# Kernel optimization log

Measured on AMD Instinct MI355X. Metric: run time of the kernel, lower is better.

## Reference

```python
import jax, jax.numpy as jnp
import numpy as np
import math

SEQ, BATCH, IN_DIM = 2048, 2, 512
EMBED, HEADS = 512, 8
HEAD_DIM = EMBED // HEADS


def setup_inputs() -> dict:
    key = jax.random.key(0)
    ks = jax.random.split(key, 6)
    # xavier-uniform style init for weights (stored as [in, out])
    def xavier(k, fan_in, fan_out):
        limit = math.sqrt(6.0 / (fan_in + fan_out))
        return jax.random.uniform(k, (fan_in, fan_out), jnp.float32, -limit, limit)
    return {
        "x": jax.random.normal(ks[0], (SEQ, BATCH, IN_DIM), jnp.float32),
        "relative_positional_bias": jax.random.normal(ks[1], (1, HEADS, SEQ, SEQ), jnp.float32),
        "Wqkv": xavier(ks[2], IN_DIM, 3 * EMBED),
        "bqkv": jnp.zeros((3 * EMBED,), jnp.float32),
        "Wo": xavier(ks[3], EMBED, EMBED),
        "bo": jnp.zeros((EMBED,), jnp.float32),
    }


def reference(x, relative_positional_bias, Wqkv, bqkv, Wo, bo):
    # x: [S, B, D] -> [B, S, D]
    xb = jnp.transpose(x, (1, 0, 2))
    B, S, _ = xb.shape
    qkv = xb @ Wqkv + bqkv                       # [B, S, 3E]
    qkv = qkv.reshape(B, S, HEADS, 3 * HEAD_DIM).transpose(0, 2, 1, 3)  # [B,H,S,3hd]
    q, k, v = jnp.split(qkv, 3, axis=-1)         # each [B, H, S, hd]
    # nonstandard scaling: 1/sqrt(2 * d_k)
    scale = 1.0 / math.sqrt(2.0 * HEAD_DIM)
    logits = jnp.einsum("bhqd,bhkd->bhqk", q, k) * scale
    logits = logits + relative_positional_bias   # broadcast over batch
    attn = jax.nn.softmax(logits, axis=-1)
    vals = jnp.einsum("bhqk,bhkd->bhqd", attn, v)  # [B, H, S, hd]
    vals = vals.transpose(0, 2, 1, 3).reshape(B, S, EMBED)
    return vals @ Wo + bo                        # [B, S, E]
```

## Files before the change

### kernel.cpp

```cpp
#include <hip/hip_runtime.h>
#include <hip/hip_bf16.h>

#define SEQ 2048
#define BATCH 2
#define IN_DIM 512
#define EMBED 512
#define HEADS 8
#define HD 64
#define N3 1536

using f32x4 = __attribute__((ext_vector_type(4))) float;
using s16x8 = __attribute__((ext_vector_type(8))) short;

__device__ __forceinline__ unsigned short f2bf(float f) {
    union { float f; unsigned int u; } v; v.f = f;
    unsigned int u = v.u;
    unsigned int r = (u + 0x7FFFu + ((u >> 16) & 1u)) >> 16;
    return (unsigned short)r;
}

__global__ __launch_bounds__(256) void prep_x(
    const float* __restrict__ x, unsigned short* __restrict__ Ab)
{
    const int gid = blockIdx.x * 256 + threadIdx.x;
    const int base = gid * 4;
    const int m = base >> 9, k = base & 511;
    const int b = m >> 11, s = m & 2047;
    float4 f = *reinterpret_cast<const float4*>(x + ((size_t)s * BATCH + b) * IN_DIM + k);
    ushort4 u;
    u.x = f2bf(f.x); u.y = f2bf(f.y); u.z = f2bf(f.z); u.w = f2bf(f.w);
    *reinterpret_cast<ushort4*>(Ab + (size_t)m * IN_DIM + k) = u;
}

__global__ __launch_bounds__(256) void transpose_w(
    const float* __restrict__ in, unsigned short* __restrict__ out, int K, int N)
{
    __shared__ __align__(16) unsigned short T[64][72];
    const int k0 = blockIdx.x * 64, n0 = blockIdx.y * 64;
    const int tid = threadIdx.x;
    const int ri = tid >> 2, cj = (tid & 3) * 16;
#pragma unroll
    for (int v = 0; v < 4; v++) {
        float4 f = *reinterpret_cast<const float4*>(in + (size_t)(k0 + ri) * N + n0 + cj + 4 * v);
        T[cj + 4 * v + 0][ri] = f2bf(f.x);
        T[cj + 4 * v + 1][ri] = f2bf(f.y);
        T[cj + 4 * v + 2][ri] = f2bf(f.z);
        T[cj + 4 * v + 3][ri] = f2bf(f.w);
    }
    __syncthreads();
    unsigned short* dst = out + (size_t)(n0 + ri) * K + k0 + cj;
    *reinterpret_cast<uint4*>(dst)     = *reinterpret_cast<const uint4*>(&T[ri][cj]);
    *reinterpret_cast<uint4*>(dst + 8) = *reinterpret_cast<const uint4*>(&T[ri][cj + 8]);
}

__global__ __launch_bounds__(256) void qkv_proj(
    const unsigned short* __restrict__ Ab, const unsigned short* __restrict__ Wt,
    const float* __restrict__ bqkv,
    unsigned short* __restrict__ Qb, unsigned short* __restrict__ Kb,
    unsigned short* __restrict__ Vt)
{
    __shared__ __align__(16) unsigned short As[64][72];
    __shared__ __align__(16) unsigned short Bs[64][72];
    const int bm = blockIdx.x, bn = blockIdx.y;
    const int tid = threadIdx.x;
    const int lane = tid & 63, w = tid >> 6;
    const int fr = lane & 15, fg = lane >> 4;
    const int m0 = bm * 64, n0 = bn * 64;
    const int ri = tid >> 2, cj = (tid & 3) * 16;

    f32x4 acc[4];
#pragma unroll
    for (int t = 0; t < 4; t++) acc[t] = (f32x4){0.f, 0.f, 0.f, 0.f};

    for (int k0 = 0; k0 < IN_DIM; k0 += 64) {
        const unsigned short* asrc = Ab + (size_t)(m0 + ri) * IN_DIM + k0 + cj;
        *reinterpret_cast<uint4*>(&As[ri][cj])     = *reinterpret_cast<const uint4*>(asrc);
        *reinterpret_cast<uint4*>(&As[ri][cj + 8]) = *reinterpret_cast<const uint4*>(asrc + 8);
        const unsigned short* bsrc = Wt + (size_t)(n0 + ri) * IN_DIM + k0 + cj;
        *reinterpret_cast<uint4*>(&Bs[ri][cj])     = *reinterpret_cast<const uint4*>(bsrc);
        *reinterpret_cast<uint4*>(&Bs[ri][cj + 8]) = *reinterpret_cast<const uint4*>(bsrc + 8);
        __syncthreads();
#pragma unroll
        for (int h2 = 0; h2 < 2; h2++) {
            s16x8 a = *reinterpret_cast<const s16x8*>(&As[w * 16 + fr][h2 * 32 + fg * 8]);
#pragma unroll
            for (int t = 0; t < 4; t++) {
                s16x8 b = *reinterpret_cast<const s16x8*>(&Bs[t * 16 + fr][h2 * 32 + fg * 8]);
                acc[t] = __builtin_amdgcn_mfma_f32_16x16x32_bf16(a, b, acc[t], 0, 0, 0);
            }
        }
        __syncthreads();
    }

    const int h = bn / 3, route = bn % 3;
    const int b_ = m0 >> 11, s0 = m0 & 2047;
    if (route < 2) {
        unsigned short* dst = (route == 0) ? Qb : Kb;
#pragma unroll
        for (int t = 0; t < 4; t++) {
            const int d = t * 16 + fr;
            const float bq = bqkv[n0 + t * 16 + fr];
#pragma unroll
            for (int j = 0; j < 4; j++) {
                const int sl = s0 + w * 16 + fg * 4 + j;
                dst[(((size_t)b_ * HEADS + h) * SEQ + sl) * HD + d] = f2bf(acc[t][j] + bq);
            }
        }
    } else {
#pragma unroll
        for (int t = 0; t < 4; t++) {
            const float bq = bqkv[n0 + t * 16 + fr];
#pragma unroll
            for (int j = 0; j < 4; j++)
                As[t * 16 + fr][w * 16 + fg * 4 + j] = f2bf(acc[t][j] + bq);
        }
        __syncthreads();
        unsigned short* dst = Vt + (((size_t)b_ * HEADS + h) * HD + ri) * SEQ + s0 + cj;
        *reinterpret_cast<uint4*>(dst)     = *reinterpret_cast<const uint4*>(&As[ri][cj]);
        *reinterpret_cast<uint4*>(dst + 8) = *reinterpret_cast<const uint4*>(&As[ri][cj + 8]);
    }
}

__global__ __launch_bounds__(256) void flash_attn(
    const unsigned short* __restrict__ Qb, const unsigned short* __restrict__ Kb,
    const unsigned short* __restrict__ Vt, const float* __restrict__ bias,
    unsigned short* __restrict__ Ob)
{
    __shared__ __align__(16) unsigned short Ks[2][64][72];
    __shared__ __align__(16) unsigned short Vs[2][64][72];
    __shared__ __align__(16) unsigned short Ps[4][16][72];
    const int h = blockIdx.y, b = blockIdx.z;
    const int q0 = blockIdx.x * 64;
    const int tid = threadIdx.x, lane = tid & 63, w = tid >> 6;
    const int fr = lane & 15, fg = lane >> 4;

    const unsigned short* Kbase = Kb + (size_t)(b * HEADS + h) * SEQ * HD;
    const unsigned short* Vbase = Vt + (size_t)(b * HEADS + h) * HD * SEQ;
    const float* bbase = bias + (size_t)h * SEQ * SEQ + (size_t)q0 * SEQ;

    const unsigned short* qrow = Qb + ((size_t)(b * HEADS + h) * SEQ + q0 + w * 16 + fr) * HD;
    s16x8 qf0 = *reinterpret_cast<const s16x8*>(qrow + fg * 8);
    s16x8 qf1 = *reinterpret_cast<const s16x8*>(qrow + 32 + fg * 8);

    const int r0 = tid >> 3, c0 = (tid & 7) * 8;
    const int r1 = r0 + 32;

    uint4 kr0, kr1, vr0, vr1;
    float bA[4][4], bB[4][4];

    kr0 = *reinterpret_cast<const uint4*>(Kbase + (size_t)r0 * HD + c0);
    kr1 = *reinterpret_cast<const uint4*>(Kbase + (size_t)r1 * HD + c0);
    vr0 = *reinterpret_cast<const uint4*>(Vbase + (size_t)r0 * SEQ + c0);
    vr1 = *reinterpret_cast<const uint4*>(Vbase + (size_t)r1 * SEQ + c0);
#pragma unroll
    for (int t = 0; t < 4; t++)
#pragma unroll
        for (int j = 0; j < 4; j++)
            bA[t][j] = bbase[(size_t)(w * 16 + fg * 4 + j) * SEQ + t * 16 + fr];
    *reinterpret_cast<uint4*>(&Ks[0][r0][c0]) = kr0;
    *reinterpret_cast<uint4*>(&Ks[0][r1][c0]) = kr1;
    *reinterpret_cast<uint4*>(&Vs[0][r0][c0]) = vr0;
    *reinterpret_cast<uint4*>(&Vs[0][r1][c0]) = vr1;
    __syncthreads();

    float mrow[4], lrow[4];
    f32x4 oacc[4];
#pragma unroll
    for (int j = 0; j < 4; j++) { mrow[j] = -1e30f; lrow[j] = 0.f; }
#pragma unroll
    for (int t = 0; t < 4; t++) oacc[t] = (f32x4){0.f, 0.f, 0.f, 0.f};

    const float scale = 0.08838834764831845f;

    auto body = [&](int n, const float (&bc)[4][4], float (&bnx)[4][4]) {
        const int cur = n & 1;
        const bool pf = (n < 31);
        const int kn = (n + 1) * 64;
        if (pf) {
            kr0 = *reinterpret_cast<const uint4*>(Kbase + (size_t)(kn + r0) * HD + c0);
            kr1 = *reinterpret_cast<const uint4*>(Kbase + (size_t)(kn + r1) * HD + c0);
            vr0 = *reinterpret_cast<const uint4*>(Vbase + (size_t)r0 * SEQ + kn + c0);
            vr1 = *reinterpret_cast<const uint4*>(Vbase + (size_t)r1 * SEQ + kn + c0);
#pragma unroll
            for (int t = 0; t < 4; t++)
#pragma unroll
                for (int j = 0; j < 4; j++)
                    bnx[t][j] = bbase[(size_t)(w * 16 + fg * 4 + j) * SEQ + kn + t * 16 + fr];
        }
        f32x4 sacc[4];
#pragma unroll
        for (int t = 0; t < 4; t++) sacc[t] = (f32x4){0.f, 0.f, 0.f, 0.f};
#pragma unroll
        for (int h2 = 0; h2 < 2; h2++) {
            s16x8 a = (h2 == 0) ? qf0 : qf1;
#pragma unroll
            for (int t = 0; t < 4; t++) {
                s16x8 kf = *reinterpret_cast<const s16x8*>(&Ks[cur][t * 16 + fr][h2 * 32 + fg * 8]);
                sacc[t] = __builtin_amdgcn_mfma_f32_16x16x32_bf16(a, kf, sacc[t], 0, 0, 0);
            }
        }
#pragma unroll
        for (int t = 0; t < 4; t++)
#pragma unroll
            for (int j = 0; j < 4; j++)
                sacc[t][j] = sacc[t][j] * scale + bc[t][j];
        float fac[4];
#pragma unroll
        for (int j = 0; j < 4; j++) {
            float m = fmaxf(fmaxf(sacc[0][j], sacc[1][j]), fmaxf(sacc[2][j], sacc[3][j]));
#pragma unroll
            for (int msk = 1; msk < 16; msk <<= 1) m = fmaxf(m, __shfl_xor(m, msk, 64));
            const float newm = fmaxf(mrow[j], m);
            fac[j] = __expf(mrow[j] - newm);
            mrow[j] = newm;
        }
#pragma unroll
        for (int t = 0; t < 4; t++)
#pragma unroll
            for (int j = 0; j < 4; j++)
                sacc[t][j] = __expf(sacc[t][j] - mrow[j]);
#pragma unroll
        for (int j = 0; j < 4; j++) {
            float s = sacc[0][j] + sacc[1][j] + sacc[2][j] + sacc[3][j];
#pragma unroll
            for (int msk = 1; msk < 16; msk <<= 1) s += __shfl_xor(s, msk, 64);
            lrow[j] = lrow[j] * fac[j] + s;
        }
#pragma unroll
        for (int t = 0; t < 4; t++)
#pragma unroll
            for (int j = 0; j < 4; j++)
                Ps[w][fg * 4 + j][t * 16 + fr] = f2bf(sacc[t][j]);
#pragma unroll
        for (int t = 0; t < 4; t++)
#pragma unroll
            for (int j = 0; j < 4; j++)
                oacc[t][j] *= fac[j];
#pragma unroll
        for (int h2 = 0; h2 < 2; h2++) {
            s16x8 pa = *reinterpret_cast<const s16x8*>(&Ps[w][fr][h2 * 32 + fg * 8]);
#pragma unroll
            for (int t = 0; t < 4; t++) {
                s16x8 vf = *reinterpret_cast<const s16x8*>(&Vs[cur][t * 16 + fr][h2 * 32 + fg * 8]);
                oacc[t] = __builtin_amdgcn_mfma_f32_16x16x32_bf16(pa, vf, oacc[t], 0, 0, 0);
            }
        }
        if (pf) {
            const int nxt = cur ^ 1;
            *reinterpret_cast<uint4*>(&Ks[nxt][r0][c0]) = kr0;
            *reinterpret_cast<uint4*>(&Ks[nxt][r1][c0]) = kr1;
            *reinterpret_cast<uint4*>(&Vs[nxt][r0][c0]) = vr0;
            *reinterpret_cast<uint4*>(&Vs[nxt][r1][c0]) = vr1;
        }
        __syncthreads();
    };

    for (int n = 0; n < 32; n += 2) {
        body(n, bA, bB);
        body(n + 1, bB, bA);
    }

#pragma unroll
    for (int t = 0; t < 4; t++)
#pragma unroll
        for (int j = 0; j < 4; j++) {
            const int grow = q0 + w * 16 + fg * 4 + j;
            const float o = oacc[t][j] / lrow[j];
            Ob[((size_t)b * SEQ + grow) * EMBED + h * HD + t * 16 + fr] = f2bf(o);
        }
}

__global__ __launch_bounds__(256) void out_proj(
    const unsigned short* __restrict__ Ao, const unsigned short* __restrict__ Wot,
    const float* __restrict__ bo, float* __restrict__ out)
{
    __shared__ __align__(16) unsigned short As[64][72];
    __shared__ __align__(16) unsigned short Bs[64][72];
    const int bm = blockIdx.x, bn = blockIdx.y;
    const int tid = threadIdx.x, lane = tid & 63, w = tid >> 6;
    const int fr = lane & 15, fg = lane >> 4;
    const int m0 = bm * 64, n0 = bn * 64;
    const int ri = tid >> 2, cj = (tid & 3) * 16;

    f32x4 acc[4];
#pragma unroll
    for (int t = 0; t < 4; t++) acc[t] = (f32x4){0.f, 0.f, 0.f, 0.f};

    for (int k0 = 0; k0 < EMBED; k0 += 64) {
        const unsigned short* asrc = Ao + (size_t)(m0 + ri) * EMBED + k0 + cj;
        *reinterpret_cast<uint4*>(&As[ri][cj])     = *reinterpret_cast<const uint4*>(asrc);
        *reinterpret_cast<uint4*>(&As[ri][cj + 8]) = *reinterpret_cast<const uint4*>(asrc + 8);
        const unsigned short* bsrc = Wot + (size_t)(n0 + ri) * EMBED + k0 + cj;
        *reinterpret_cast<uint4*>(&Bs[ri][cj])     = *reinterpret_cast<const uint4*>(bsrc);
        *reinterpret_cast<uint4*>(&Bs[ri][cj + 8]) = *reinterpret_cast<const uint4*>(bsrc + 8);
        __syncthreads();
#pragma unroll
        for (int h2 = 0; h2 < 2; h2++) {
            s16x8 a = *reinterpret_cast<const s16x8*>(&As[w * 16 + fr][h2 * 32 + fg * 8]);
#pragma unroll
            for (int t = 0; t < 4; t++) {
                s16x8 b = *reinterpret_cast<const s16x8*>(&Bs[t * 16 + fr][h2 * 32 + fg * 8]);
                acc[t] = __builtin_amdgcn_mfma_f32_16x16x32_bf16(a, b, acc[t], 0, 0, 0);
            }
        }
        __syncthreads();
    }

#pragma unroll
    for (int t = 0; t < 4; t++) {
        const int col = n0 + t * 16 + fr;
        const float bb = bo[col];
#pragma unroll
        for (int j = 0; j < 4; j++) {
            const int grow = m0 + w * 16 + fg * 4 + j;
            out[(size_t)grow * EMBED + col] = acc[t][j] + bb;
        }
    }
}

extern "C" void kernel_launch(void* const* d_in, const int* in_sizes, int n_in,
                              void* d_out, int out_size, void* d_ws, size_t ws_size,
                              hipStream_t stream) {
    const float* x    = (const float*)d_in[0];
    const float* bias = (const float*)d_in[1];
    const float* Wqkv = (const float*)d_in[2];
    const float* bqkv = (const float*)d_in[3];
    const float* Wo   = (const float*)d_in[4];
    const float* bo   = (const float*)d_in[5];
    float* out = (float*)d_out;

    const size_t perT = (size_t)BATCH * HEADS * SEQ * HD;
    unsigned short* Qb    = (unsigned short*)d_ws;
    unsigned short* Kb    = Qb + perT;
    unsigned short* Vt    = Kb + perT;
    unsigned short* Ob    = Vt + perT;
    unsigned short* Ab    = Ob + perT;
    unsigned short* Wqkvt = Ab + (size_t)BATCH * SEQ * IN_DIM;
    unsigned short* Wot   = Wqkvt + (size_t)N3 * IN_DIM;

    prep_x<<<2048, 256, 0, stream>>>(x, Ab);
    transpose_w<<<dim3(8, 24), 256, 0, stream>>>(Wqkv, Wqkvt, IN_DIM, N3);
    transpose_w<<<dim3(8, 8), 256, 0, stream>>>(Wo, Wot, EMBED, EMBED);
    qkv_proj<<<dim3(64, 24), 256, 0, stream>>>(Ab, Wqkvt, bqkv, Qb, Kb, Vt);
    flash_attn<<<dim3(32, 8, 2), 256, 0, stream>>>(Qb, Kb, Vt, bias, Ob);
    out_proj<<<dim3(64, 8), 256, 0, stream>>>(Ob, Wot, bo, out);
}
```

Before: 266.1 us.

## Split attention KV range across blocks, async-LDS GEMMs, transposed score MFMA

Flash attention can now split the key range in two, doubling the grid, and a combine kernel merges the partial outputs using the saved row max and sum. The score and PV MFMAs swap operands so each lane owns one query row, which allows vectorised bias loads and cuts the shuffle reductions. The QKV and output GEMMs move to 64x128 tiles filled with global_load_lds and an XOR-swizzled LDS layout, and the two weight transposes merge into one launch. The split path runs only when the workspace is large enough, and it adds fp32 partial traffic plus an extra kernel launch.

```diff
diff --git a/kernel.cpp b/kernel.cpp
--- a/kernel.cpp
+++ b/kernel.cpp
@@ -17,6 +17,12 @@
     unsigned int u = v.u;
     unsigned int r = (u + 0x7FFFu + ((u >> 16) & 1u)) >> 16;
     return (unsigned short)r;
+}
+
+__device__ __forceinline__ void async16(void* lds, const void* g) {
+    __builtin_amdgcn_global_load_lds(
+        (const __attribute__((address_space(1))) unsigned int*)g,
+        (__attribute__((address_space(3))) unsigned int*)lds, 16, 0, 0);
 }
 
 __global__ __launch_bounds__(256) void prep_x(
@@ -32,11 +38,16 @@
     *reinterpret_cast<ushort4*>(Ab + (size_t)m * IN_DIM + k) = u;
 }
 
-__global__ __launch_bounds__(256) void transpose_w(
-    const float* __restrict__ in, unsigned short* __restrict__ out, int K, int N)
+__global__ __launch_bounds__(256) void transpose_w2(
+    const float* __restrict__ Wqkv, const float* __restrict__ Wo,
+    unsigned short* __restrict__ Wqkvt, unsigned short* __restrict__ Wot)
 {
     __shared__ __align__(16) unsigned short T[64][72];
-    const int k0 = blockIdx.x * 64, n0 = blockIdx.y * 64;
+    const int yy = blockIdx.y;
+    const float* in; unsigned short* out; int N, n0;
+    if (yy < 24) { in = Wqkv; out = Wqkvt; N = N3;    n0 = yy * 64; }
+    else         { in = Wo;   out = Wot;   N = EMBED; n0 = (yy - 24) * 64; }
+    const int k0 = blockIdx.x * 64;
     const int tid = threadIdx.x;
     const int ri = tid >> 2, cj = (tid & 3) * 16;
 #pragma unroll
@@ -48,88 +59,120 @@
         T[cj + 4 * v + 3][ri] = f2bf(f.w);
     }
     __syncthreads();
-    unsigned short* dst = out + (size_t)(n0 + ri) * K + k0 + cj;
+    unsigned short* dst = out + (size_t)(n0 + ri) * IN_DIM + k0 + cj;
     *reinterpret_cast<uint4*>(dst)     = *reinterpret_cast<const uint4*>(&T[ri][cj]);
     *reinterpret_cast<uint4*>(dst + 8) = *reinterpret_cast<const uint4*>(&T[ri][cj + 8]);
 }
 
-__global__ __launch_bounds__(256) void qkv_proj(
+__global__ __launch_bounds__(256) void qkv_gemm(
     const unsigned short* __restrict__ Ab, const unsigned short* __restrict__ Wt,
     const float* __restrict__ bqkv,
     unsigned short* __restrict__ Qb, unsigned short* __restrict__ Kb,
     unsigned short* __restrict__ Vt)
 {
-    __shared__ __align__(16) unsigned short As[64][72];
-    __shared__ __align__(16) unsigned short Bs[64][72];
-    const int bm = blockIdx.x, bn = blockIdx.y;
-    const int tid = threadIdx.x;
-    const int lane = tid & 63, w = tid >> 6;
+    __shared__ __align__(16) unsigned short As[64 * 64];
+    __shared__ __align__(16) unsigned short Bs[128 * 64];
+    const int tid = threadIdx.x, lane = tid & 63, w = tid >> 6;
     const int fr = lane & 15, fg = lane >> 4;
-    const int m0 = bm * 64, n0 = bn * 64;
-    const int ri = tid >> 2, cj = (tid & 3) * 16;
-
-    f32x4 acc[4];
-#pragma unroll
-    for (int t = 0; t < 4; t++) acc[t] = (f32x4){0.f, 0.f, 0.f, 0.f};
+    const int m0 = blockIdx.x * 64, n0 = blockIdx.y * 128;
+    const int sr = lane >> 3;
+    const int scs = ((lane & 7) * 16) ^ (sr << 4);
+
+    const unsigned char* Ag = (const unsigned char*)Ab + (size_t)(m0 + w * 8 + sr) * 1024 + scs;
+    const unsigned char* Bg = (const unsigned char*)Wt + (size_t)(n0 + w * 8 + sr) * 1024 + scs;
+    unsigned char* Asb = (unsigned char*)As;
+    unsigned char* Bsb = (unsigned char*)Bs;
+
+    f32x4 acc[2][4];
+#pragma unroll
+    for (int mt = 0; mt < 2; mt++)
+#pragma unroll
+        for (int nt = 0; nt < 4; nt++) acc[mt][nt] = (f32x4){0.f, 0.f, 0.f, 0.f};
+
+    const int swz = (fr & 7) << 4;
 
     for (int k0 = 0; k0 < IN_DIM; k0 += 64) {
-        const unsigned short* asrc = Ab + (size_t)(m0 + ri) * IN_DIM + k0 + cj;
-        *reinterpret_cast<uint4*>(&As[ri][cj])     = *reinterpret_cast<const uint4*>(asrc);
-        *reinterpret_cast<uint4*>(&As[ri][cj + 8]) = *reinterpret_cast<const uint4*>(asrc + 8);
-        const unsigned short* bsrc = Wt + (size_t)(n0 + ri) * IN_DIM + k0 + cj;
-        *reinterpret_cast<uint4*>(&Bs[ri][cj])     = *reinterpret_cast<const uint4*>(bsrc);
-        *reinterpret_cast<uint4*>(&Bs[ri][cj + 8]) = *reinterpret_cast<const uint4*>(bsrc + 8);
+        async16(Asb + (w * 8) * 128,        Ag);
+        async16(Asb + (32 + w * 8) * 128,   Ag + (size_t)32 * 1024);
+        async16(Bsb + (w * 8) * 128,        Bg);
+        async16(Bsb + (32 + w * 8) * 128,   Bg + (size_t)32 * 1024);
+        async16(Bsb + (64 + w * 8) * 128,   Bg + (size_t)64 * 1024);
+        async16(Bsb + (96 + w * 8) * 128,   Bg + (size_t)96 * 1024);
+        Ag += 128; Bg += 128;
         __syncthreads();
 #pragma unroll
         for (int h2 = 0; h2 < 2; h2++) {
-            s16x8 a = *reinterpret_cast<const s16x8*>(&As[w * 16 + fr][h2 * 32 + fg * 8]);
-#pragma unroll
-            for (int t = 0; t < 4; t++) {
-                s16x8 b = *reinterpret_cast<const s16x8*>(&Bs[t * 16 + fr][h2 * 32 + fg * 8]);
-                acc[t] = __builtin_amdgcn_mfma_f32_16x16x32_bf16(a, b, acc[t], 0, 0, 0);
-            }
+            const int cb = (h2 * 64 + fg * 16) ^ swz;
+            s16x8 a[2], bf[4];
+#pragma unroll
+            for (int mt = 0; mt < 2; mt++) {
+                const int row = (w >> 1) * 32 + mt * 16 + fr;
+                a[mt] = *reinterpret_cast<const s16x8*>(Asb + row * 128 + cb);
+            }
+#pragma unroll
+            for (int nt = 0; nt < 4; nt++) {
+                const int nrow = (w & 1) * 64 + nt * 16 + fr;
+                bf[nt] = *reinterpret_cast<const s16x8*>(Bsb + nrow * 128 + cb);
+            }
+#pragma unroll
+            for (int mt = 0; mt < 2; mt++)
+#pragma unroll
+                for (int nt = 0; nt < 4; nt++)
+                    acc[mt][nt] = __builtin_amdgcn_mfma_f32_16x16x32_bf16(a[mt], bf[nt], acc[mt][nt], 0, 0, 0);
         }
         __syncthreads();
     }
 
-    const int h = bn / 3, route = bn % 3;
-    const int b_ = m0 >> 11, s0 = m0 & 2047;
-    if (route < 2) {
-        unsigned short* dst = (route == 0) ? Qb : Kb;
-#pragma unroll
-        for (int t = 0; t < 4; t++) {
-            const int d = t * 16 + fr;
-            const float bq = bqkv[n0 + t * 16 + fr];
-#pragma unroll
-            for (int j = 0; j < 4; j++) {
-                const int sl = s0 + w * 16 + fg * 4 + j;
-                dst[(((size_t)b_ * HEADS + h) * SEQ + sl) * HD + d] = f2bf(acc[t][j] + bq);
-            }
-        }
-    } else {
-#pragma unroll
-        for (int t = 0; t < 4; t++) {
-            const float bq = bqkv[n0 + t * 16 + fr];
-#pragma unroll
-            for (int j = 0; j < 4; j++)
-                As[t * 16 + fr][w * 16 + fg * 4 + j] = f2bf(acc[t][j] + bq);
-        }
-        __syncthreads();
-        unsigned short* dst = Vt + (((size_t)b_ * HEADS + h) * HD + ri) * SEQ + s0 + cj;
-        *reinterpret_cast<uint4*>(dst)     = *reinterpret_cast<const uint4*>(&As[ri][cj]);
-        *reinterpret_cast<uint4*>(dst + 8) = *reinterpret_cast<const uint4*>(&As[ri][cj + 8]);
-    }
-}
-
+    const int wc = w & 1, wr = w >> 1;
+    const int b_ = m0 >> 11;
+    const int sB = (m0 & 2047) + wr * 32;
+#pragma unroll
+    for (int nt = 0; nt < 4; nt++) {
+        const int col0 = n0 + wc * 64 + nt * 16;
+        const int g = col0 >> 6;
+        const int hh = g / 3, part = g % 3;
+        const int d = (col0 & 63) + fr;
+        const float bq = bqkv[col0 + fr];
+        if (part < 2) {
+            unsigned short* dst = (part == 0 ? Qb : Kb) + ((size_t)b_ * HEADS + hh) * SEQ * HD;
+#pragma unroll
+            for (int mt = 0; mt < 2; mt++)
+#pragma unroll
+                for (int j = 0; j < 4; j++) {
+                    const int s = sB + mt * 16 + fg * 4 + j;
+                    dst[(size_t)s * HD + d] = f2bf(acc[mt][nt][j] + bq);
+                }
+        } else {
+            unsigned short* dst = Vt + (((size_t)b_ * HEADS + hh) * HD + d) * SEQ;
+#pragma unroll
+            for (int mt = 0; mt < 2; mt++) {
+                ushort4 u;
+                u.x = f2bf(acc[mt][nt][0] + bq);
+                u.y = f2bf(acc[mt][nt][1] + bq);
+                u.z = f2bf(acc[mt][nt][2] + bq);
+                u.w = f2bf(acc[mt][nt][3] + bq);
+                *reinterpret_cast<ushort4*>(&dst[sB + mt * 16 + fg * 4]) = u;
+            }
+        }
+    }
+}
+
+template<int NSPL>
 __global__ __launch_bounds__(256) void flash_attn(
     const unsigned short* __restrict__ Qb, const unsigned short* __restrict__ Kb,
     const unsigned short* __restrict__ Vt, const float* __restrict__ bias,
-    unsigned short* __restrict__ Ob)
+    unsigned short* __restrict__ Ob, float* __restrict__ Opart,
+    float* __restrict__ Mpart, float* __restrict__ Lpart)
 {
     __shared__ __align__(16) unsigned short Ks[2][64][72];
     __shared__ __align__(16) unsigned short Vs[2][64][72];
     __shared__ __align__(16) unsigned short Ps[4][16][72];
-    const int h = blockIdx.y, b = blockIdx.z;
+    const int h = blockIdx.y;
+    const int z = blockIdx.z;
+    const int b  = (NSPL == 2) ? (z >> 1) : z;
+    const int sp = (NSPL == 2) ? (z & 1) : 0;
+    const int NST = (NSPL == 2) ? 16 : 32;
+    const int kst = sp * (SEQ / NSPL);
     const int q0 = blockIdx.x * 64;
     const int tid = threadIdx.x, lane = tid & 63, w = tid >> 6;
     const int fr = lane & 15, fg = lane >> 4;
@@ -146,36 +189,33 @@
     const int r1 = r0 + 32;
 
     uint4 kr0, kr1, vr0, vr1;
-    float bA[4][4], bB[4][4];
-
-    kr0 = *reinterpret_cast<const uint4*>(Kbase + (size_t)r0 * HD + c0);
-    kr1 = *reinterpret_cast<const uint4*>(Kbase + (size_t)r1 * HD + c0);
-    vr0 = *reinterpret_cast<const uint4*>(Vbase + (size_t)r0 * SEQ + c0);
-    vr1 = *reinterpret_cast<const uint4*>(Vbase + (size_t)r1 * SEQ + c0);
+    f32x4 bA[4], bB[4];
+    const float* brow = bbase + (size_t)(w * 16 + fr) * SEQ;
+
+    kr0 = *reinterpret_cast<const uint4*>(Kbase + (size_t)(kst + r0) * HD + c0);
+    kr1 = *reinterpret_cast<const uint4*>(Kbase + (size_t)(kst + r1) * HD + c0);
+    vr0 = *reinterpret_cast<const uint4*>(Vbase + (size_t)r0 * SEQ + kst + c0);
+    vr1 = *reinterpret_cast<const uint4*>(Vbase + (size_t)r1 * SEQ + kst + c0);
 #pragma unroll
     for (int t = 0; t < 4; t++)
-#pragma unroll
-        for (int j = 0; j < 4; j++)
-            bA[t][j] = bbase[(size_t)(w * 16 + fg * 4 + j) * SEQ + t * 16 + fr];
+        bA[t] = *reinterpret_cast<const f32x4*>(brow + kst + t * 16 + fg * 4);
     *reinterpret_cast<uint4*>(&Ks[0][r0][c0]) = kr0;
     *reinterpret_cast<uint4*>(&Ks[0][r1][c0]) = kr1;
     *reinterpret_cast<uint4*>(&Vs[0][r0][c0]) = vr0;
     *reinterpret_cast<uint4*>(&Vs[0][r1][c0]) = vr1;
     __syncthreads();
 
-    float mrow[4], lrow[4];
+    float mrow = -1e30f, lrow = 0.f;
     f32x4 oacc[4];
 #pragma unroll
-    for (int j = 0; j < 4; j++) { mrow[j] = -1e30f; lrow[j] = 0.f; }
-#pragma unroll
     for (int t = 0; t < 4; t++) oacc[t] = (f32x4){0.f, 0.f, 0.f, 0.f};
 
     const float scale = 0.08838834764831845f;
 
-    auto body = [&](int n, const float (&bc)[4][4], float (&bnx)[4][4]) {
+    auto body = [&](int n, const f32x4 (&bc)[4], f32x4 (&bnx)[4]) {
         const int cur = n & 1;
-        const bool pf = (n < 31);
-        const int kn = (n + 1) * 64;
+        const bool pf = (n < NST - 1);
+        const int kn = kst + (n + 1) * 64;
         if (pf) {
             kr0 = *reinterpret_cast<const uint4*>(Kbase + (size_t)(kn + r0) * HD + c0);
             kr1 = *reinterpret_cast<const uint4*>(Kbase + (size_t)(kn + r1) * HD + c0);
@@ -183,66 +223,62 @@
             vr1 = *reinterpret_cast<const uint4*>(Vbase + (size_t)r1 * SEQ + kn + c0);
 #pragma unroll
             for (int t = 0; t < 4; t++)
-#pragma unroll
-                for (int j = 0; j < 4; j++)
-                    bnx[t][j] = bbase[(size_t)(w * 16 + fg * 4 + j) * SEQ + kn + t * 16 + fr];
-        }
-        f32x4 sacc[4];
-#pragma unroll
-        for (int t = 0; t < 4; t++) sacc[t] = (f32x4){0.f, 0.f, 0.f, 0.f};
+                bnx[t] = *reinterpret_cast<const f32x4*>(brow + kn + t * 16 + fg * 4);
+        }
+        f32x4 p[4];
+#pragma unroll
+        for (int t = 0; t < 4; t++) p[t] = (f32x4){0.f, 0.f, 0.f, 0.f};
 #pragma unroll
         for (int h2 = 0; h2 < 2; h2++) {
-            s16x8 a = (h2 == 0) ? qf0 : qf1;
+            s16x8 qf = (h2 == 0) ? qf0 : qf1;
 #pragma unroll
             for (int t = 0; t < 4; t++) {
                 s16x8 kf = *reinterpret_cast<const s16x8*>(&Ks[cur][t * 16 + fr][h2 * 32 + fg * 8]);
-                sacc[t] = __builtin_amdgcn_mfma_f32_16x16x32_bf16(a, kf, sacc[t], 0, 0, 0);
+                p[t] = __builtin_amdgcn_mfma_f32_16x16x32_bf16(kf, qf, p[t], 0, 0, 0);
             }
         }
 #pragma unroll
         for (int t = 0; t < 4; t++)
 #pragma unroll
             for (int j = 0; j < 4; j++)
-                sacc[t][j] = sacc[t][j] * scale + bc[t][j];
-        float fac[4];
-#pragma unroll
-        for (int j = 0; j < 4; j++) {
-            float m = fmaxf(fmaxf(sacc[0][j], sacc[1][j]), fmaxf(sacc[2][j], sacc[3][j]));
-#pragma unroll
-            for (int msk = 1; msk < 16; msk <<= 1) m = fmaxf(m, __shfl_xor(m, msk, 64));
-            const float newm = fmaxf(mrow[j], m);
-            fac[j] = __expf(mrow[j] - newm);
-            mrow[j] = newm;
-        }
+                p[t][j] = p[t][j] * scale + bc[t][j];
+        float tm = fmaxf(fmaxf(fmaxf(p[0][0], p[0][1]), fmaxf(p[0][2], p[0][3])),
+                         fmaxf(fmaxf(p[1][0], p[1][1]), fmaxf(p[1][2], p[1][3])));
+        tm = fmaxf(tm, fmaxf(fmaxf(fmaxf(p[2][0], p[2][1]), fmaxf(p[2][2], p[2][3])),
+                             fmaxf(fmaxf(p[3][0], p[3][1]), fmaxf(p[3][2], p[3][3]))));
+        tm = fmaxf(tm, __shfl_xor(tm, 16, 64));
+        tm = fmaxf(tm, __shfl_xor(tm, 32, 64));
+        const float newm = fmaxf(mrow, tm);
+        const float fac = __expf(mrow - newm);
+        mrow = newm;
 #pragma unroll
         for (int t = 0; t < 4; t++)
 #pragma unroll
             for (int j = 0; j < 4; j++)
-                sacc[t][j] = __expf(sacc[t][j] - mrow[j]);
-#pragma unroll
-        for (int j = 0; j < 4; j++) {
-            float s = sacc[0][j] + sacc[1][j] + sacc[2][j] + sacc[3][j];
-#pragma unroll
-            for (int msk = 1; msk < 16; msk <<= 1) s += __shfl_xor(s, msk, 64);
-            lrow[j] = lrow[j] * fac[j] + s;
+                p[t][j] = __expf(p[t][j] - mrow);
+        float ts = (p[0][0] + p[0][1] + p[0][2] + p[0][3]) + (p[1][0] + p[1][1] + p[1][2] + p[1][3])
+                 + (p[2][0] + p[2][1] + p[2][2] + p[2][3]) + (p[3][0] + p[3][1] + p[3][2] + p[3][3]);
+        ts += __shfl_xor(ts, 16, 64);
+        ts += __shfl_xor(ts, 32, 64);
+        lrow = lrow * fac + ts;
+#pragma unroll
+        for (int t = 0; t < 4; t++) {
+            ushort4 u;
+            u.x = f2bf(p[t][0]); u.y = f2bf(p[t][1]); u.z = f2bf(p[t][2]); u.w = f2bf(p[t][3]);
+            *reinterpret_cast<ushort4*>(&Ps[w][fr][t * 16 + fg * 4]) = u;
         }
 #pragma unroll
         for (int t = 0; t < 4; t++)
 #pragma unroll
             for (int j = 0; j < 4; j++)
-                Ps[w][fg * 4 + j][t * 16 + fr] = f2bf(sacc[t][j]);
-#pragma unroll
-        for (int t = 0; t < 4; t++)
-#pragma unroll
-            for (int j = 0; j < 4; j++)
-                oacc[t][j] *= fac[j];
+                oacc[t][j] *= fac;
 #pragma unroll
         for (int h2 = 0; h2 < 2; h2++) {
             s16x8 pa = *reinterpret_cast<const s16x8*>(&Ps[w][fr][h2 * 32 + fg * 8]);
 #pragma unroll
             for (int t = 0; t < 4; t++) {
                 s16x8 vf = *reinterpret_cast<const s16x8*>(&Vs[cur][t * 16 + fr][h2 * 32 + fg * 8]);
-                oacc[t] = __builtin_amdgcn_mfma_f32_16x16x32_bf16(pa, vf, oacc[t], 0, 0, 0);
+                oacc[t] = __builtin_amdgcn_mfma_f32_16x16x32_bf16(vf, pa, oacc[t], 0, 0, 0);
             }
         }
         if (pf) {
@@ -255,66 +291,133 @@
         __syncthreads();
     };
 
-    for (int n = 0; n < 32; n += 2) {
+    for (int n = 0; n < NST; n += 2) {
         body(n, bA, bB);
         body(n + 1, bB, bA);
     }
 
-#pragma unroll
-    for (int t = 0; t < 4; t++)
-#pragma unroll
-        for (int j = 0; j < 4; j++) {
-            const int grow = q0 + w * 16 + fg * 4 + j;
-            const float o = oacc[t][j] / lrow[j];
-            Ob[((size_t)b * SEQ + grow) * EMBED + h * HD + t * 16 + fr] = f2bf(o);
-        }
-}
-
-__global__ __launch_bounds__(256) void out_proj(
+    if (NSPL == 1) {
+        const float inv = 1.f / lrow;
+        unsigned short* dst = Ob + ((size_t)b * SEQ + q0 + w * 16 + fr) * EMBED + h * HD;
+#pragma unroll
+        for (int t = 0; t < 4; t++) {
+            ushort4 u;
+            u.x = f2bf(oacc[t][0] * inv); u.y = f2bf(oacc[t][1] * inv);
+            u.z = f2bf(oacc[t][2] * inv); u.w = f2bf(oacc[t][3] * inv);
+            *reinterpret_cast<ushort4*>(dst + t * 16 + fg * 4) = u;
+        }
+    } else {
+        const int tile = (z * HEADS + h) * 32 + blockIdx.x;
+        float* Op = Opart + (size_t)tile * 4096 + (w * 16 + fr) * 64;
+#pragma unroll
+        for (int t = 0; t < 4; t++)
+            *reinterpret_cast<f32x4*>(Op + t * 16 + fg * 4) = oacc[t];
+        if (fg == 0) {
+            Mpart[tile * 64 + w * 16 + fr] = mrow;
+            Lpart[tile * 64 + w * 16 + fr] = lrow;
+        }
+    }
+}
+
+__global__ __launch_bounds__(256) void combine(
+    const float* __restrict__ Opart, const float* __restrict__ Mpart,
+    const float* __restrict__ Lpart, unsigned short* __restrict__ Ob)
+{
+    const int qt = blockIdx.x, h = blockIdx.y, b = blockIdx.z;
+    const int t = threadIdx.x;
+    const int q = t >> 2, dc = (t & 3) * 16;
+    const int t0 = ((b * 2 + 0) * HEADS + h) * 32 + qt;
+    const int t1 = ((b * 2 + 1) * HEADS + h) * 32 + qt;
+    const float m1 = Mpart[t0 * 64 + q], l1 = Lpart[t0 * 64 + q];
+    const float m2 = Mpart[t1 * 64 + q], l2 = Lpart[t1 * 64 + q];
+    const float M = fmaxf(m1, m2);
+    const float w1 = __expf(m1 - M), w2 = __expf(m2 - M);
+    const float inv = 1.f / (w1 * l1 + w2 * l2);
+    const float* o1 = Opart + (size_t)t0 * 4096 + q * 64 + dc;
+    const float* o2 = Opart + (size_t)t1 * 4096 + q * 64 + dc;
+    unsigned short* dst = Ob + ((size_t)b * SEQ + qt * 64 + q) * EMBED + h * HD + dc;
+#pragma unroll
+    for (int v = 0; v < 4; v++) {
+        f32x4 a = *reinterpret_cast<const f32x4*>(o1 + 4 * v);
+        f32x4 c = *reinterpret_cast<const f32x4*>(o2 + 4 * v);
+        ushort4 u;
+        u.x = f2bf((w1 * a[0] + w2 * c[0]) * inv);
+        u.y = f2bf((w1 * a[1] + w2 * c[1]) * inv);
+        u.z = f2bf((w1 * a[2] + w2 * c[2]) * inv);
+        u.w = f2bf((w1 * a[3] + w2 * c[3]) * inv);
+        *reinterpret_cast<ushort4*>(dst + 4 * v) = u;
+    }
+}
+
+__global__ __launch_bounds__(256) void out_gemm(
     const unsigned short* __restrict__ Ao, const unsigned short* __restrict__ Wot,
     const float* __restrict__ bo, float* __restrict__ out)
 {
-    __shared__ __align__(16) unsigned short As[64][72];
-    __shared__ __align__(16) unsigned short Bs[64][72];
-    const int bm = blockIdx.x, bn = blockIdx.y;
+    __shared__ __align__(16) unsigned short As[64 * 64];
+    __shared__ __align__(16) unsigned short Bs[128 * 64];
     const int tid = threadIdx.x, lane = tid & 63, w = tid >> 6;
     const int fr = lane & 15, fg = lane >> 4;
-    const int m0 = bm * 64, n0 = bn * 64;
-    const int ri = tid >> 2, cj = (tid & 3) * 16;
-
-    f32x4 acc[4];
-#pragma unroll
-    for (int t = 0; t < 4; t++) acc[t] = (f32x4){0.f, 0.f, 0.f, 0.f};
+    const int m0 = blockIdx.x * 64, n0 = blockIdx.y * 128;
+    const int sr = lane >> 3;
+    const int scs = ((lane & 7) * 16) ^ (sr << 4);
+
+    const unsigned char* Ag = (const unsigned char*)Ao  + (size_t)(m0 + w * 8 + sr) * 1024 + scs;
+    const unsigned char* Bg = (const unsigned char*)Wot + (size_t)(n0 + w * 8 + sr) * 1024 + scs;
+    unsigned char* Asb = (unsigned char*)As;
+    unsigned char* Bsb = (unsigned char*)Bs;
+
+    f32x4 acc[2][4];
+#pragma unroll
+    for (int mt = 0; mt < 2; mt++)
+#pragma unroll
+        for (int nt = 0; nt < 4; nt++) acc[mt][nt] = (f32x4){0.f, 0.f, 0.f, 0.f};
+
+    const int swz = (fr & 7) << 4;
 
     for (int k0 = 0; k0 < EMBED; k0 += 64) {
-        const unsigned short* asrc = Ao + (size_t)(m0 + ri) * EMBED + k0 + cj;
-        *reinterpret_cast<uint4*>(&As[ri][cj])     = *reinterpret_cast<const uint4*>(asrc);
-        *reinterpret_cast<uint4*>(&As[ri][cj + 8]) = *reinterpret_cast<const uint4*>(asrc + 8);
-        const unsigned short* bsrc = Wot + (size_t)(n0 + ri) * EMBED + k0 + cj;
-        *reinterpret_cast<uint4*>(&Bs[ri][cj])     = *reinterpret_cast<const uint4*>(bsrc);
-        *reinterpret_cast<uint4*>(&Bs[ri][cj + 8]) = *reinterpret_cast<const uint4*>(bsrc + 8);
+        async16(Asb + (w * 8) * 128,        Ag);
+        async16(Asb + (32 + w * 8) * 128,   Ag + (size_t)32 * 1024);
+        async16(Bsb + (w * 8) * 128,        Bg);
+        async16(Bsb + (32 + w * 8) * 128,   Bg + (size_t)32 * 1024);
+        async16(Bsb + (64 + w * 8) * 128,   Bg + (size_t)64 * 1024);
+        async16(Bsb + (96 + w * 8) * 128,   Bg + (size_t)96 * 1024);
+        Ag += 128; Bg += 128;
         __syncthreads();
 #pragma unroll
         for (int h2 = 0; h2 < 2; h2++) {
-            s16x8 a = *reinterpret_cast<const s16x8*>(&As[w * 16 + fr][h2 * 32 + fg * 8]);
-#pragma unroll
-            for (int t = 0; t < 4; t++) {
-                s16x8 b = *reinterpret_cast<const s16x8*>(&Bs[t * 16 + fr][h2 * 32 + fg * 8]);
-                acc[t] = __builtin_amdgcn_mfma_f32_16x16x32_bf16(a, b, acc[t], 0, 0, 0);
-            }
+            const int cb = (h2 * 64 + fg * 16) ^ swz;
+            s16x8 a[2], bf[4];
+#pragma unroll
+            for (int mt = 0; mt < 2; mt++) {
+                const int row = (w >> 1) * 32 + mt * 16 + fr;
+                a[mt] = *reinterpret_cast<const s16x8*>(Asb + row * 128 + cb);
+            }
+#pragma unroll
+            for (int nt = 0; nt < 4; nt++) {
+                const int nrow = (w & 1) * 64 + nt * 16 + fr;
+                bf[nt] = *reinterpret_cast<const s16x8*>(Bsb + nrow * 128 + cb);
+            }
+#pragma unroll
+            for (int mt = 0; mt < 2; mt++)
+#pragma unroll
+                for (int nt = 0; nt < 4; nt++)
+                    acc[mt][nt] = __builtin_amdgcn_mfma_f32_16x16x32_bf16(a[mt], bf[nt], acc[mt][nt], 0, 0, 0);
         }
         __syncthreads();
     }
 
-#pragma unroll
-    for (int t = 0; t < 4; t++) {
-        const int col = n0 + t * 16 + fr;
+    const int wc = w & 1, wr = w >> 1;
+#pragma unroll
+    for (int nt = 0; nt < 4; nt++) {
+        const int col = n0 + wc * 64 + nt * 16 + fr;
         const float bb = bo[col];
 #pragma unroll
-        for (int j = 0; j < 4; j++) {
-            const int grow = m0 + w * 16 + fg * 4 + j;
-            out[(size_t)grow * EMBED + col] = acc[t][j] + bb;
-        }
+        for (int mt = 0; mt < 2; mt++)
+#pragma unroll
+            for (int j = 0; j < 4; j++) {
+                const int m = m0 + wr * 32 + mt * 16 + fg * 4 + j;
+                out[(size_t)m * EMBED + col] = acc[mt][nt][j] + bb;
+            }
     }
 }
 
@@ -337,11 +440,21 @@
     unsigned short* Ab    = Ob + perT;
     unsigned short* Wqkvt = Ab + (size_t)BATCH * SEQ * IN_DIM;
     unsigned short* Wot   = Wqkvt + (size_t)N3 * IN_DIM;
+    const size_t base_bytes = (size_t)(5 * perT + (size_t)N3 * IN_DIM + (size_t)EMBED * EMBED) * 2;
+    float* Opart = (float*)((unsigned char*)d_ws + base_bytes);
+    float* Mpart = Opart + (size_t)4 * HEADS * 32 * 4096;
+    float* Lpart = Mpart + (size_t)4 * HEADS * 32 * 64;
+    const size_t need = base_bytes + ((size_t)4 * HEADS * 32 * 4096 + (size_t)2 * 4 * HEADS * 32 * 64) * 4;
+    const bool split = (ws_size >= need);
 
     prep_x<<<2048, 256, 0, stream>>>(x, Ab);
-    transpose_w<<<dim3(8, 24), 256, 0, stream>>>(Wqkv, Wqkvt, IN_DIM, N3);
-    transpose_w<<<dim3(8, 8), 256, 0, stream>>>(Wo, Wot, EMBED, EMBED);
-    qkv_proj<<<dim3(64, 24), 256, 0, stream>>>(Ab, Wqkvt, bqkv, Qb, Kb, Vt);
-    flash_attn<<<dim3(32, 8, 2), 256, 0, stream>>>(Qb, Kb, Vt, bias, Ob);
-    out_proj<<<dim3(64, 8), 256, 0, stream>>>(Ob, Wot, bo, out);
-}
+    transpose_w2<<<dim3(8, 32), 256, 0, stream>>>(Wqkv, Wo, Wqkvt, Wot);
+    qkv_gemm<<<dim3(64, 12), 256, 0, stream>>>(Ab, Wqkvt, bqkv, Qb, Kb, Vt);
+    if (split) {
+        flash_attn<2><<<dim3(32, 8, 4), 256, 0, stream>>>(Qb, Kb, Vt, bias, Ob, Opart, Mpart, Lpart);
+        combine<<<dim3(32, 8, 2), 256, 0, stream>>>(Opart, Mpart, Lpart, Ob);
+    } else {
+        flash_attn<1><<<dim3(32, 8, 2), 256, 0, stream>>>(Qb, Kb, Vt, bias, Ob, Opart, Mpart, Lpart);
+    }
+    out_gemm<<<dim3(64, 4), 256, 0, stream>>>(Ob, Wot, bo, out);
+}
```

Result: no change. 269.9 us (+1.4%).
